# Kernel tuning notes

Measured on AMD Instinct MI355X. Metric: run time of the kernel, lower is better.

Reference implementation:

```python
import jax, jax.numpy as jnp
import numpy as np

FEATURE_SIZE = 128
STRIDE = 16
BASE_SIZE = 16
RATIOS = [0.5, 1, 2]
SCALES = [8, 16, 32]


def _generate_anchors(feature_size, stride):
    # Faithful to the torch module's numpy anchor generation (incl. rounding).
    size = BASE_SIZE * BASE_SIZE
    size_ratios = size / np.array(RATIOS)
    ws = np.round(np.sqrt(size_ratios))
    hs = np.round(ws * np.array(RATIOS))
    base = []
    for w, h in zip(ws, hs):
        for s in SCALES:
            base.append([0.0, 0.0, w * s, h * s])
    base = np.array(base)  # [9, 4]
    xo, yo = np.meshgrid(np.arange(feature_size), np.arange(feature_size), indexing='ij')
    # original loop order: x outer, y inner, then 9 base anchors
    centers = np.stack([xo * stride, yo * stride], axis=-1).reshape(-1, 1, 2)  # [F*F,1,2]
    wh = np.broadcast_to(base[None, :, 2:4], (feature_size * feature_size, 9, 2))
    anchors = np.concatenate([np.broadcast_to(centers, wh.shape), wh], axis=-1).reshape(-1, 4)
    return jnp.asarray(anchors, dtype=jnp.float32)  # [F*F*9, 4]


def _conv(x, w, b, pad):
    y = jax.lax.conv_general_dilated(
        x, w, window_strides=(1, 1), padding=[(pad, pad), (pad, pad)],
        dimension_numbers=('NCHW', 'OIHW', 'NCHW'))
    return y + b[None, :, None, None]


def setup_inputs() -> dict:
    key = jax.random.key(0)
    ks = jax.random.split(key, 4)
    F = FEATURE_SIZE
    x = jax.random.normal(ks[0], (1, 1024, F, F), dtype=jnp.float32)
    base_w = jax.random.normal(ks[1], (512, 1024, 3, 3), dtype=jnp.float32) * 0.01
    base_b = jnp.zeros((512,), dtype=jnp.float32)
    cls_w = jax.random.normal(ks[2], (18, 512, 1, 1), dtype=jnp.float32) * 0.01
    cls_b = jnp.zeros((18,), dtype=jnp.float32)
    reg_w = jax.random.normal(ks[3], (36, 512, 1, 1), dtype=jnp.float32) * 0.01
    reg_b = jnp.zeros((36,), dtype=jnp.float32)
    return {"x": x, "base_w": base_w, "base_b": base_b,
            "cls_w": cls_w, "cls_b": cls_b, "reg_w": reg_w, "reg_b": reg_b}


def reference(x, base_w, base_b, cls_w, cls_b, reg_w, reg_b):
    F = FEATURE_SIZE
    anchors = _generate_anchors(F, STRIDE)  # [N,4], N = F*F*9

    rpn_conv = jax.nn.relu(_conv(x, base_w, base_b, pad=1))        # [1,512,F,F]
    rpn_cls = _conv(rpn_conv, cls_w, cls_b, pad=0)                  # [1,18,F,F]
    # softmax over the 2-way fg/bg axis after reshape, as in the original
    cls_rs = rpn_cls.reshape(1, 2, 9 * F, F)
    cls_prob = jax.nn.softmax(cls_rs, axis=1).reshape(1, 18, F, F)
    rpn_reg = _conv(rpn_conv, reg_w, reg_b, pad=0)                  # [1,36,F,F]

    cls = jnp.transpose(cls_prob, (0, 2, 3, 1)).reshape(-1, 2)      # [N,2]
    reg = jnp.transpose(rpn_reg, (0, 2, 3, 1)).reshape(-1, 4)       # [N,4]

    # Vectorized decode — faithful to the original per-anchor loop math:
    # p0 = ax + aw*d0 ; p1 = ay + ah*d1 ; p2 = aw + exp(d2) ; p3 = ah + exp(d3)
    p0 = anchors[:, 0] + anchors[:, 2] * reg[:, 0]
    p1 = anchors[:, 1] + anchors[:, 3] * reg[:, 1]
    p2 = anchors[:, 2] + jnp.exp(reg[:, 2])
    p3 = anchors[:, 3] + jnp.exp(reg[:, 3])
    proposals = jnp.stack([p0, p1, p2, p3], axis=-1)                # [N,4]
    scores = cls[:, 1]                                              # [N]
    return jnp.concatenate([proposals, scores[:, None]], axis=-1)   # [N,5]
```

## Files before the change

kernel.cpp:

```cpp
#include <hip/hip_runtime.h>
#include <hip/hip_bf16.h>

typedef unsigned short u16;
typedef short s8v __attribute__((ext_vector_type(8)));
typedef float f4v __attribute__((ext_vector_type(4)));

#define F 128
#define CIN 1024
#define CMID 512
#define XP 130
#define K9 9216

#define A_ELEMS 8704
#define B_ELEMS 8192
#define AOFF(b) ((b) * A_ELEMS)
#define BOFF(b) (2 * A_ELEMS + (b) * B_ELEMS)

__device__ __forceinline__ u16 f2bf(float v) {
    union { float f; unsigned u; } x; x.f = v;
    unsigned r = x.u + 0x7fff + ((x.u >> 16) & 1);
    return (u16)(r >> 16);
}
__device__ __forceinline__ float bf2f(u16 u) {
    union { unsigned u; float f; } x; x.u = ((unsigned)u) << 16; return x.f;
}

__device__ __forceinline__ void gl16(const u16* g, u16* l) {
    __builtin_amdgcn_global_load_lds(
        (const __attribute__((address_space(1))) void*)g,
        (__attribute__((address_space(3))) void*)l,
        16, 0, 0);
}

__constant__ float WBASE[9] = {184.f, 368.f, 736.f, 128.f, 256.f, 512.f,  88.f, 176.f, 352.f};
__constant__ float HBASE[9] = { 96.f, 192.f, 384.f, 128.f, 256.f, 512.f, 176.f, 352.f, 704.f};

__global__ __launch_bounds__(256) void prep_all(
    const float* __restrict__ x, const float* __restrict__ bw,
    const float* __restrict__ cls_w, const float* __restrict__ reg_w,
    u16* __restrict__ xpad, u16* __restrict__ wt, u16* __restrict__ wc) {
    __shared__ char ldsraw[18624];
    const int b = blockIdx.x;
    const int tid = threadIdx.x;

    if (b < 258) {
        int t = b * 256 + tid;
        int cell = t >> 7, c8 = (t & 127) * 8;
        int h, w;
        if (cell < 130)      { h = 0;   w = cell; }
        else if (cell < 260) { h = 129; w = cell - 130; }
        else { int rm = cell - 260; h = 1 + (rm >> 1); w = (rm & 1) * 129; }
        s8v z = {};
        *(s8v*)&xpad[(h * XP + w) * CIN + c8] = z;
    } else if (b < 4354) {
        float (*lds)[65] = (float(*)[65])ldsraw;
        const int b2 = b - 258;
        const int h  = b2 >> 5;
        const int w0 = ((b2 >> 4) & 1) * 64;
        const int c0 = (b2 & 15) * 64;
        {
            const int wl = tid & 63, ci = tid >> 6;
            #pragma unroll
            for (int k = 0; k < 16; ++k) {
                int cl = ci * 16 + k;
                lds[cl][wl] = x[(c0 + cl) * (F * F) + h * F + (w0 + wl)];
            }
        }
        __syncthreads();
        {
            const int cs = (tid & 7) * 8;
            #pragma unroll
            for (int pass = 0; pass < 2; ++pass) {
                const int wl = (tid >> 3) + pass * 32;
                s8v v;
                #pragma unroll
                for (int j = 0; j < 8; ++j) v[j] = (short)f2bf(lds[cs + j][wl]);
                *(s8v*)&xpad[((h + 1) * XP + (w0 + wl + 1)) * CIN + c0 + cs] = v;
            }
        }
    } else if (b < 4866) {
        u16* lds = (u16*)ldsraw;
        const int oc = b - 4354;
        for (int k = 0; k < 36; ++k) {
            int idx = k * 256 + tid;
            float v = bw[oc * K9 + idx];
            int c = idx / 9, q = idx - c * 9;
            lds[q * 1033 + c] = f2bf(v);
        }
        __syncthreads();
        for (int k = 0; k < 36; ++k) {
            int idx = k * 256 + tid;
            int q = idx >> 10, c = idx & 1023;
            wt[oc * K9 + idx] = lds[q * 1033 + c];
        }
    } else {
        int t = (b - 4866) * 256 + tid;
        int oc = t >> 9, c = t & 511;
        float v = 0.f;
        if (oc < 18)      v = cls_w[oc * 512 + c];
        else if (oc < 54) v = reg_w[(oc - 18) * 512 + c];
        wc[t] = f2bf(v);
    }
}

__global__ __launch_bounds__(256, 2) void gemm_conv(
    const u16* __restrict__ xpad, const u16* __restrict__ wt,
    const float* __restrict__ bias, u16* __restrict__ rpn) {
    __shared__ u16 smem[2 * A_ELEMS + 2 * B_ELEMS];
    const int tid = threadIdx.x;
    const int bid = blockIdx.x;
    const int oc0 = ((bid & 7) >> 1) * 128;
    const int gh  = (bid >> 3) * 2 + (bid & 1);

    const int lane = tid & 63;
    const int wv = tid >> 6;
    const int lm = lane & 15;
    const int lq = lane >> 4;
    const int wm = (wv >> 1) * 64;
    const int wn = (wv & 1) * 64;

    const int sw = (lane & 7) ^ ((lane >> 3) & 7);
    const u16* pA = xpad + (lane >> 3) * CIN + sw * 8;
    const u16* pB = wt + (size_t)(oc0 + wv * 32 + (lane >> 3)) * K9 + sw * 8;

    f4v acc[4][4] = {};

    auto issueA = [&](int ms) {
        const int dy = ms >> 4, cc = ms & 15;
        const u16* src = pA + ((gh + dy) * XP) * CIN + cc * 64;
        u16* dst = &smem[AOFF(ms & 1)];
        #pragma unroll
        for (int jj = 0; jj < 4; ++jj) {
            const int ci = wv * 4 + jj;
            gl16(src + ci * 8 * CIN, dst + ci * 512);
        }
        if (wv == 0) gl16(src + 16 * 8 * CIN, dst + 16 * 512);
    };
    auto issueB = [&](int ms, int dx, int buf) {
        const int dy = ms >> 4, cc = ms & 15;
        const int dydx = dy * 3 + dx;
        const u16* src = pB + dydx * CIN + cc * 64;
        u16* dst = &smem[BOFF(buf) + wv * 32 * 64];
        #pragma unroll
        for (int jj = 0; jj < 4; ++jj)
            gl16(src + jj * 8 * K9, dst + jj * 8 * 64);
    };

    issueA(0);
    issueB(0, 0, 0);
    __syncthreads();

    int t = 0;
    for (int ms = 0; ms < 48; ++ms) {
        const u16* Ab = &smem[AOFF(ms & 1)];
        #pragma unroll
        for (int dx = 0; dx < 3; ++dx, ++t) {
            if (t + 1 < 144) {
                const int msn = (dx == 2) ? ms + 1 : ms;
                const int dxn = (dx == 2) ? 0 : dx + 1;
                issueB(msn, dxn, (t + 1) & 1);
            }
            if (dx == 0 && ms + 1 < 48) issueA(ms + 1);
            const u16* Bb = &smem[BOFF(t & 1)];
            #pragma unroll
            for (int kk = 0; kk < 2; ++kk) {
                const int kseg = kk * 4 + lq;
                s8v af[4], bfr[4];
                #pragma unroll
                for (int i = 0; i < 4; ++i) {
                    const int ra = wm + i * 16 + lm + dx;
                    const int rb = wn + i * 16 + lm;
                    af[i]  = *(const s8v*)&Ab[ra * 64 + ((kseg ^ (ra & 7)) << 3)];
                    bfr[i] = *(const s8v*)&Bb[rb * 64 + ((kseg ^ (rb & 7)) << 3)];
                }
                #pragma unroll
                for (int mi = 0; mi < 4; ++mi)
                    #pragma unroll
                    for (int ni = 0; ni < 4; ++ni)
                        acc[mi][ni] = __builtin_amdgcn_mfma_f32_16x16x32_bf16(
                            af[mi], bfr[ni], acc[mi][ni], 0, 0, 0);
            }
            __syncthreads();
        }
    }

    #pragma unroll
    for (int ni = 0; ni < 4; ++ni) {
        const int oc = oc0 + wn + ni * 16 + lm;
        const float bv = bias[oc];
        #pragma unroll
        for (int mi = 0; mi < 4; ++mi) {
            #pragma unroll
            for (int rr = 0; rr < 4; ++rr) {
                const int m = wm + mi * 16 + lq * 4 + rr;
                float v = acc[mi][ni][rr] + bv;
                v = v > 0.f ? v : 0.f;
                rpn[(gh * 128 + m) * CMID + oc] = f2bf(v);
            }
        }
    }
}

__global__ __launch_bounds__(256) void stage23(
    const u16* __restrict__ rpn, const u16* __restrict__ wc,
    const float* __restrict__ cls_b, const float* __restrict__ reg_b,
    float* __restrict__ out) {
    __shared__ float vals[64][65];
    const int tid = threadIdx.x, lane = tid & 63, wv = tid >> 6;
    const int lm = lane & 15, lq = lane >> 4;
    const int m0 = blockIdx.x * 64 + wv * 16;
    f4v acc[4] = {};
    const u16* arow = rpn + (m0 + lm) * CMID + lq * 8;
    const u16* brow = wc + lm * CMID + lq * 8;
    #pragma unroll
    for (int k = 0; k < 16; ++k) {
        s8v af = *(const s8v*)(arow + k * 32);
        #pragma unroll
        for (int ni = 0; ni < 4; ++ni) {
            s8v bf = *(const s8v*)(brow + ni * 16 * CMID + k * 32);
            acc[ni] = __builtin_amdgcn_mfma_f32_16x16x32_bf16(af, bf, acc[ni], 0, 0, 0);
        }
    }
    #pragma unroll
    for (int ni = 0; ni < 4; ++ni) {
        const int ch = ni * 16 + lm;
        const float bv = ch < 18 ? cls_b[ch] : (ch < 54 ? reg_b[ch - 18] : 0.f);
        #pragma unroll
        for (int rr = 0; rr < 4; ++rr)
            vals[wv * 16 + lq * 4 + rr][ch] = acc[ni][rr] + bv;
    }
    __syncthreads();
    const int pbase = blockIdx.x * 64;
    for (int q = tid; q < 576; q += 256) {
        const int pl = q / 9, a = q - pl * 9;
        const float* v = vals[pl];
        const int ch = 2 * a + 1;
        const int pair = (ch < 9) ? ch + 9 : ch - 9;
        const float score = 1.f / (1.f + expf(v[pair] - v[ch]));
        const float r0 = v[18 + 4 * a], r1 = v[19 + 4 * a];
        const float r2 = v[20 + 4 * a], r3 = v[21 + 4 * a];
        const float wb = WBASE[a], hb = HBASE[a];
        const int p = pbase + pl;
        const int h = p >> 7, w = p & 127;
        float* o = out + (p * 9 + a) * 5;
        o[0] = h * 16.f + wb * r0;
        o[1] = w * 16.f + hb * r1;
        o[2] = wb + expf(r2);
        o[3] = hb + expf(r3);
        o[4] = score;
    }
}

extern "C" void kernel_launch(void* const* d_in, const int* in_sizes, int n_in,
                              void* d_out, int out_size, void* d_ws, size_t ws_size,
                              hipStream_t stream) {
    const float* x      = (const float*)d_in[0];
    const float* base_w = (const float*)d_in[1];
    const float* base_b = (const float*)d_in[2];
    const float* cls_w  = (const float*)d_in[3];
    const float* cls_b  = (const float*)d_in[4];
    const float* reg_w  = (const float*)d_in[5];
    const float* reg_b  = (const float*)d_in[6];
    float* out = (float*)d_out;

    char* ws = (char*)d_ws;
    u16* xpad = (u16*)ws;
    u16* wt   = (u16*)(ws + 34611200);
    u16* wc   = (u16*)(ws + 34611200 + 9437184);
    u16* rpn  = (u16*)(ws + 34611200 + 9437184 + 65536);

    prep_all<<<4994, 256, 0, stream>>>(x, base_w, cls_w, reg_w, xpad, wt, wc);
    gemm_conv<<<512, 256, 0, stream>>>(xpad, wt, base_b, rpn);
    stage23<<<256, 256, 0, stream>>>(rpn, wc, cls_b, reg_b, out);
}
```

Baseline: 276.4 us.

## Load GEMM weight fragments directly from global memory, dropping LDS staging for B

The conv GEMM stops staging weight tiles in shared memory. Each lane now reads its B fragments straight from global memory into registers. This removes the B double buffer and cuts the barriers from three per input slice to one, and the smaller LDS footprint lets launch bounds rise to three blocks per SU. The input transpose prep kernel also switches to 16-byte vectorized float4 reads. The cost is that weight loads now sit on the critical path with global latency and no reuse across waves, and the higher occupancy target may force register spills.

```diff
diff --git a/kernel.cpp b/kernel.cpp
--- a/kernel.cpp
+++ b/kernel.cpp
@@ -12,9 +12,7 @@
 #define K9 9216
 
 #define A_ELEMS 8704
-#define B_ELEMS 8192
 #define AOFF(b) ((b) * A_ELEMS)
-#define BOFF(b) (2 * A_ELEMS + (b) * B_ELEMS)
 
 __device__ __forceinline__ u16 f2bf(float v) {
     union { float f; unsigned u; } x; x.f = v;
@@ -59,11 +57,14 @@
         const int w0 = ((b2 >> 4) & 1) * 64;
         const int c0 = (b2 & 15) * 64;
         {
-            const int wl = tid & 63, ci = tid >> 6;
-            #pragma unroll
-            for (int k = 0; k < 16; ++k) {
-                int cl = ci * 16 + k;
-                lds[cl][wl] = x[(c0 + cl) * (F * F) + h * F + (w0 + wl)];
+            const int c  = tid >> 2;
+            const int wq = tid & 3;
+            const float* src = x + (c0 + c) * (F * F) + h * F + w0 + wq * 16;
+            #pragma unroll
+            for (int k = 0; k < 4; ++k) {
+                f4v v = *(const f4v*)(src + k * 4);
+                #pragma unroll
+                for (int j = 0; j < 4; ++j) lds[c][wq * 16 + k * 4 + j] = v[j];
             }
         }
         __syncthreads();
@@ -103,10 +104,10 @@
     }
 }
 
-__global__ __launch_bounds__(256, 2) void gemm_conv(
+__global__ __launch_bounds__(256, 3) void gemm_conv(
     const u16* __restrict__ xpad, const u16* __restrict__ wt,
     const float* __restrict__ bias, u16* __restrict__ rpn) {
-    __shared__ u16 smem[2 * A_ELEMS + 2 * B_ELEMS];
+    __shared__ u16 smem[2 * A_ELEMS];
     const int tid = threadIdx.x;
     const int bid = blockIdx.x;
     const int oc0 = ((bid & 7) >> 1) * 128;
@@ -121,7 +122,7 @@
 
     const int sw = (lane & 7) ^ ((lane >> 3) & 7);
     const u16* pA = xpad + (lane >> 3) * CIN + sw * 8;
-    const u16* pB = wt + (size_t)(oc0 + wv * 32 + (lane >> 3)) * K9 + sw * 8;
+    const u16* pB = wt + (size_t)(oc0 + wn + lm) * K9 + lq * 8;
 
     f4v acc[4][4] = {};
 
@@ -136,42 +137,29 @@
         }
         if (wv == 0) gl16(src + 16 * 8 * CIN, dst + 16 * 512);
     };
-    auto issueB = [&](int ms, int dx, int buf) {
+
+    issueA(0);
+    __syncthreads();
+
+    for (int ms = 0; ms < 48; ++ms) {
         const int dy = ms >> 4, cc = ms & 15;
-        const int dydx = dy * 3 + dx;
-        const u16* src = pB + dydx * CIN + cc * 64;
-        u16* dst = &smem[BOFF(buf) + wv * 32 * 64];
-        #pragma unroll
-        for (int jj = 0; jj < 4; ++jj)
-            gl16(src + jj * 8 * K9, dst + jj * 8 * 64);
-    };
-
-    issueA(0);
-    issueB(0, 0, 0);
-    __syncthreads();
-
-    int t = 0;
-    for (int ms = 0; ms < 48; ++ms) {
+        if (ms + 1 < 48) issueA(ms + 1);
         const u16* Ab = &smem[AOFF(ms & 1)];
-        #pragma unroll
-        for (int dx = 0; dx < 3; ++dx, ++t) {
-            if (t + 1 < 144) {
-                const int msn = (dx == 2) ? ms + 1 : ms;
-                const int dxn = (dx == 2) ? 0 : dx + 1;
-                issueB(msn, dxn, (t + 1) & 1);
-            }
-            if (dx == 0 && ms + 1 < 48) issueA(ms + 1);
-            const u16* Bb = &smem[BOFF(t & 1)];
+        const u16* pBm = pB + (dy * 3) * CIN + cc * 64;
+        #pragma unroll
+        for (int dx = 0; dx < 3; ++dx) {
+            const u16* pBd = pBm + dx * CIN;
             #pragma unroll
             for (int kk = 0; kk < 2; ++kk) {
+                s8v af[4], bfr[4];
+                #pragma unroll
+                for (int i = 0; i < 4; ++i)
+                    bfr[i] = *(const s8v*)(pBd + (size_t)i * 16 * K9 + kk * 32);
                 const int kseg = kk * 4 + lq;
-                s8v af[4], bfr[4];
                 #pragma unroll
                 for (int i = 0; i < 4; ++i) {
                     const int ra = wm + i * 16 + lm + dx;
-                    const int rb = wn + i * 16 + lm;
-                    af[i]  = *(const s8v*)&Ab[ra * 64 + ((kseg ^ (ra & 7)) << 3)];
-                    bfr[i] = *(const s8v*)&Bb[rb * 64 + ((kseg ^ (rb & 7)) << 3)];
+                    af[i] = *(const s8v*)&Ab[ra * 64 + ((kseg ^ (ra & 7)) << 3)];
                 }
                 #pragma unroll
                 for (int mi = 0; mi < 4; ++mi)
@@ -180,8 +168,8 @@
                         acc[mi][ni] = __builtin_amdgcn_mfma_f32_16x16x32_bf16(
                             af[mi], bfr[ni], acc[mi][ni], 0, 0, 0);
             }
-            __syncthreads();
-        }
+        }
+        __syncthreads();
     }
 
     #pragma unroll
```

Measured after the change: 422.6 us. +52.9%, slower.

## Split prep kernel, vectorize x loads, and use split-K in stage23

Applied to the files above, without the earlier changes.

The fused prep kernel is split into separate x-transpose and weight-transpose kernels. This lets the x path use a smaller LDS footprint and 16-byte vectorized global loads. stage23 now splits the K=512 reduction across the 4 waves, reduces the partial sums through LDS, and launches 1024 blocks of 16 pixels instead of 256 blocks of 64, to expose more parallelism. The costs are an extra kernel launch and an extra LDS reduction with additional barriers.

```diff
diff --git a/kernel.cpp b/kernel.cpp
--- a/kernel.cpp
+++ b/kernel.cpp
@@ -35,11 +35,9 @@
 __constant__ float WBASE[9] = {184.f, 368.f, 736.f, 128.f, 256.f, 512.f,  88.f, 176.f, 352.f};
 __constant__ float HBASE[9] = { 96.f, 192.f, 384.f, 128.f, 256.f, 512.f, 176.f, 352.f, 704.f};
 
-__global__ __launch_bounds__(256) void prep_all(
-    const float* __restrict__ x, const float* __restrict__ bw,
-    const float* __restrict__ cls_w, const float* __restrict__ reg_w,
-    u16* __restrict__ xpad, u16* __restrict__ wt, u16* __restrict__ wc) {
-    __shared__ char ldsraw[18624];
+__global__ __launch_bounds__(256) void prep_x(
+    const float* __restrict__ x, u16* __restrict__ xpad) {
+    __shared__ float lds[64][65];
     const int b = blockIdx.x;
     const int tid = threadIdx.x;
 
@@ -52,35 +50,45 @@
         else { int rm = cell - 260; h = 1 + (rm >> 1); w = (rm & 1) * 129; }
         s8v z = {};
         *(s8v*)&xpad[(h * XP + w) * CIN + c8] = z;
-    } else if (b < 4354) {
-        float (*lds)[65] = (float(*)[65])ldsraw;
-        const int b2 = b - 258;
-        const int h  = b2 >> 5;
-        const int w0 = ((b2 >> 4) & 1) * 64;
-        const int c0 = (b2 & 15) * 64;
-        {
-            const int wl = tid & 63, ci = tid >> 6;
-            #pragma unroll
-            for (int k = 0; k < 16; ++k) {
-                int cl = ci * 16 + k;
-                lds[cl][wl] = x[(c0 + cl) * (F * F) + h * F + (w0 + wl)];
-            }
-        }
-        __syncthreads();
-        {
-            const int cs = (tid & 7) * 8;
-            #pragma unroll
-            for (int pass = 0; pass < 2; ++pass) {
-                const int wl = (tid >> 3) + pass * 32;
-                s8v v;
-                #pragma unroll
-                for (int j = 0; j < 8; ++j) v[j] = (short)f2bf(lds[cs + j][wl]);
-                *(s8v*)&xpad[((h + 1) * XP + (w0 + wl + 1)) * CIN + c0 + cs] = v;
-            }
-        }
-    } else if (b < 4866) {
-        u16* lds = (u16*)ldsraw;
-        const int oc = b - 4354;
+        return;
+    }
+    const int b2 = b - 258;
+    const int h  = b2 >> 5;
+    const int w0 = ((b2 >> 4) & 1) * 64;
+    const int c0 = (b2 & 15) * 64;
+    {
+        const int c  = tid >> 2;
+        const int wq = tid & 3;
+        const float* src = x + (c0 + c) * (F * F) + h * F + w0 + wq * 16;
+        #pragma unroll
+        for (int k = 0; k < 4; ++k) {
+            f4v v = *(const f4v*)(src + k * 4);
+            #pragma unroll
+            for (int j = 0; j < 4; ++j) lds[c][wq * 16 + k * 4 + j] = v[j];
+        }
+    }
+    __syncthreads();
+    {
+        const int cs = (tid & 7) * 8;
+        #pragma unroll
+        for (int pass = 0; pass < 2; ++pass) {
+            const int wl = (tid >> 3) + pass * 32;
+            s8v v;
+            #pragma unroll
+            for (int j = 0; j < 8; ++j) v[j] = (short)f2bf(lds[cs + j][wl]);
+            *(s8v*)&xpad[((h + 1) * XP + (w0 + wl + 1)) * CIN + c0 + cs] = v;
+        }
+    }
+}
+
+__global__ __launch_bounds__(256) void prep_w(
+    const float* __restrict__ bw, const float* __restrict__ cls_w,
+    const float* __restrict__ reg_w, u16* __restrict__ wt, u16* __restrict__ wc) {
+    __shared__ u16 lds[9 * 1033];
+    const int b = blockIdx.x;
+    const int tid = threadIdx.x;
+    if (b < 512) {
+        const int oc = b;
         for (int k = 0; k < 36; ++k) {
             int idx = k * 256 + tid;
             float v = bw[oc * K9 + idx];
@@ -94,7 +102,7 @@
             wt[oc * K9 + idx] = lds[q * 1033 + c];
         }
     } else {
-        int t = (b - 4866) * 256 + tid;
+        int t = (b - 512) * 256 + tid;
         int oc = t >> 9, c = t & 511;
         float v = 0.f;
         if (oc < 18)      v = cls_w[oc * 512 + c];
@@ -205,15 +213,16 @@
     const u16* __restrict__ rpn, const u16* __restrict__ wc,
     const float* __restrict__ cls_b, const float* __restrict__ reg_b,
     float* __restrict__ out) {
-    __shared__ float vals[64][65];
+    __shared__ float part[4][16][65];
     const int tid = threadIdx.x, lane = tid & 63, wv = tid >> 6;
     const int lm = lane & 15, lq = lane >> 4;
-    const int m0 = blockIdx.x * 64 + wv * 16;
+    const int m0 = blockIdx.x * 16;
+
     f4v acc[4] = {};
-    const u16* arow = rpn + (m0 + lm) * CMID + lq * 8;
-    const u16* brow = wc + lm * CMID + lq * 8;
-    #pragma unroll
-    for (int k = 0; k < 16; ++k) {
+    const u16* arow = rpn + (m0 + lm) * CMID + wv * 128 + lq * 8;
+    const u16* brow = wc + lm * CMID + wv * 128 + lq * 8;
+    #pragma unroll
+    for (int k = 0; k < 4; ++k) {
         s8v af = *(const s8v*)(arow + k * 32);
         #pragma unroll
         for (int ni = 0; ni < 4; ++ni) {
@@ -222,25 +231,37 @@
         }
     }
     #pragma unroll
-    for (int ni = 0; ni < 4; ++ni) {
-        const int ch = ni * 16 + lm;
-        const float bv = ch < 18 ? cls_b[ch] : (ch < 54 ? reg_b[ch - 18] : 0.f);
+    for (int ni = 0; ni < 4; ++ni)
         #pragma unroll
         for (int rr = 0; rr < 4; ++rr)
-            vals[wv * 16 + lq * 4 + rr][ch] = acc[ni][rr] + bv;
-    }
-    __syncthreads();
-    const int pbase = blockIdx.x * 64;
-    for (int q = tid; q < 576; q += 256) {
-        const int pl = q / 9, a = q - pl * 9;
-        const float* v = vals[pl];
+            part[wv][lq * 4 + rr][ni * 16 + lm] = acc[ni][rr];
+    __syncthreads();
+
+    float vsum[4];
+    const int col = tid & 63, rb = tid >> 6;
+    const float bv = col < 18 ? cls_b[col] : (col < 54 ? reg_b[col - 18] : 0.f);
+    #pragma unroll
+    for (int rr = 0; rr < 4; ++rr) {
+        const int row = rb * 4 + rr;
+        vsum[rr] = part[0][row][col] + part[1][row][col]
+                 + part[2][row][col] + part[3][row][col] + bv;
+    }
+    __syncthreads();
+    #pragma unroll
+    for (int rr = 0; rr < 4; ++rr)
+        part[0][rb * 4 + rr][col] = vsum[rr];
+    __syncthreads();
+
+    if (tid < 144) {
+        const int pl = tid / 9, a = tid - pl * 9;
+        const float* v = part[0][pl];
         const int ch = 2 * a + 1;
         const int pair = (ch < 9) ? ch + 9 : ch - 9;
         const float score = 1.f / (1.f + expf(v[pair] - v[ch]));
         const float r0 = v[18 + 4 * a], r1 = v[19 + 4 * a];
         const float r2 = v[20 + 4 * a], r3 = v[21 + 4 * a];
         const float wb = WBASE[a], hb = HBASE[a];
-        const int p = pbase + pl;
+        const int p = m0 + pl;
         const int h = p >> 7, w = p & 127;
         float* o = out + (p * 9 + a) * 5;
         o[0] = h * 16.f + wb * r0;
@@ -269,7 +290,8 @@
     u16* wc   = (u16*)(ws + 34611200 + 9437184);
     u16* rpn  = (u16*)(ws + 34611200 + 9437184 + 65536);
 
-    prep_all<<<4994, 256, 0, stream>>>(x, base_w, cls_w, reg_w, xpad, wt, wc);
+    prep_x<<<4354, 256, 0, stream>>>(x, xpad);
+    prep_w<<<640, 256, 0, stream>>>(base_w, cls_w, reg_w, wt, wc);
     gemm_conv<<<512, 256, 0, stream>>>(xpad, wt, base_b, rpn);
-    stage23<<<256, 256, 0, stream>>>(rpn, wc, cls_b, reg_b, out);
-}
+    stage23<<<1024, 256, 0, stream>>>(rpn, wc, cls_b, reg_b, out);
+}
```

After: 266.0 us. 1.04x faster.

## Fuse 1x1 head stage into conv GEMM via last-block atomic counter; vectorize x loads

Applied to the files above, without the earlier changes.

Removes the separate stage23 kernel. Each image row's four output-channel blocks bump an atomic counter, and the last one to finish runs the 1x1 cls/reg MFMA and the anchor decode for that row. Counters are zeroed by an extra block in the prep kernel. The x transpose load in prep also switches from scalar reads to float4 vector loads. The aim is to cut one launch and its tail, at the cost of serialising the head work onto the last-arriving blocks and adding threadfence/atomic overhead.

```diff
diff --git a/kernel.cpp b/kernel.cpp
--- a/kernel.cpp
+++ b/kernel.cpp
@@ -38,7 +38,8 @@
 __global__ __launch_bounds__(256) void prep_all(
     const float* __restrict__ x, const float* __restrict__ bw,
     const float* __restrict__ cls_w, const float* __restrict__ reg_w,
-    u16* __restrict__ xpad, u16* __restrict__ wt, u16* __restrict__ wc) {
+    u16* __restrict__ xpad, u16* __restrict__ wt, u16* __restrict__ wc,
+    int* __restrict__ cnt) {
     __shared__ char ldsraw[18624];
     const int b = blockIdx.x;
     const int tid = threadIdx.x;
@@ -59,11 +60,14 @@
         const int w0 = ((b2 >> 4) & 1) * 64;
         const int c0 = (b2 & 15) * 64;
         {
-            const int wl = tid & 63, ci = tid >> 6;
-            #pragma unroll
-            for (int k = 0; k < 16; ++k) {
-                int cl = ci * 16 + k;
-                lds[cl][wl] = x[(c0 + cl) * (F * F) + h * F + (w0 + wl)];
+            const int c  = tid >> 2;
+            const int wq = tid & 3;
+            const float* src = x + (c0 + c) * (F * F) + h * F + w0 + wq * 16;
+            #pragma unroll
+            for (int k = 0; k < 4; ++k) {
+                f4v v = *(const f4v*)(src + k * 4);
+                #pragma unroll
+                for (int j = 0; j < 4; ++j) lds[c][wq * 16 + k * 4 + j] = v[j];
             }
         }
         __syncthreads();
@@ -93,20 +97,26 @@
             int q = idx >> 10, c = idx & 1023;
             wt[oc * K9 + idx] = lds[q * 1033 + c];
         }
-    } else {
+    } else if (b < 4994) {
         int t = (b - 4866) * 256 + tid;
         int oc = t >> 9, c = t & 511;
         float v = 0.f;
         if (oc < 18)      v = cls_w[oc * 512 + c];
         else if (oc < 54) v = reg_w[(oc - 18) * 512 + c];
         wc[t] = f2bf(v);
+    } else {
+        if (tid < 128) cnt[tid] = 0;
     }
 }
 
 __global__ __launch_bounds__(256, 2) void gemm_conv(
     const u16* __restrict__ xpad, const u16* __restrict__ wt,
-    const float* __restrict__ bias, u16* __restrict__ rpn) {
+    const float* __restrict__ bias, u16* __restrict__ rpn,
+    const u16* __restrict__ wc, const float* __restrict__ cls_b,
+    const float* __restrict__ reg_b, float* __restrict__ out,
+    int* __restrict__ cnt) {
     __shared__ u16 smem[2 * A_ELEMS + 2 * B_ELEMS];
+    __shared__ int lastflag;
     const int tid = threadIdx.x;
     const int bid = blockIdx.x;
     const int oc0 = ((bid & 7) >> 1) * 128;
@@ -199,26 +209,25 @@
             }
         }
     }
-}
-
-__global__ __launch_bounds__(256) void stage23(
-    const u16* __restrict__ rpn, const u16* __restrict__ wc,
-    const float* __restrict__ cls_b, const float* __restrict__ reg_b,
-    float* __restrict__ out) {
-    __shared__ float vals[64][65];
-    const int tid = threadIdx.x, lane = tid & 63, wv = tid >> 6;
-    const int lm = lane & 15, lq = lane >> 4;
-    const int m0 = blockIdx.x * 64 + wv * 16;
-    f4v acc[4] = {};
-    const u16* arow = rpn + (m0 + lm) * CMID + lq * 8;
-    const u16* brow = wc + lm * CMID + lq * 8;
+
+    __threadfence();
+    if (tid == 0) lastflag = atomicAdd(&cnt[gh], 1);
+    __syncthreads();
+    if (lastflag != 3) return;
+    __threadfence();
+
+    float (*vals)[65] = (float(*)[65])smem;
+    const u16* rrow = rpn + (size_t)(gh * 128) * CMID;
+    f4v a2[2][4] = {};
     #pragma unroll
     for (int k = 0; k < 16; ++k) {
-        s8v af = *(const s8v*)(arow + k * 32);
+        s8v af0 = *(const s8v*)&rrow[(wv * 32 + lm) * CMID + k * 32 + lq * 8];
+        s8v af1 = *(const s8v*)&rrow[(wv * 32 + 16 + lm) * CMID + k * 32 + lq * 8];
         #pragma unroll
         for (int ni = 0; ni < 4; ++ni) {
-            s8v bf = *(const s8v*)(brow + ni * 16 * CMID + k * 32);
-            acc[ni] = __builtin_amdgcn_mfma_f32_16x16x32_bf16(af, bf, acc[ni], 0, 0, 0);
+            s8v bf = *(const s8v*)&wc[(ni * 16 + lm) * CMID + k * 32 + lq * 8];
+            a2[0][ni] = __builtin_amdgcn_mfma_f32_16x16x32_bf16(af0, bf, a2[0][ni], 0, 0, 0);
+            a2[1][ni] = __builtin_amdgcn_mfma_f32_16x16x32_bf16(af1, bf, a2[1][ni], 0, 0, 0);
         }
     }
     #pragma unroll
@@ -226,12 +235,13 @@
         const int ch = ni * 16 + lm;
         const float bv = ch < 18 ? cls_b[ch] : (ch < 54 ? reg_b[ch - 18] : 0.f);
         #pragma unroll
-        for (int rr = 0; rr < 4; ++rr)
-            vals[wv * 16 + lq * 4 + rr][ch] = acc[ni][rr] + bv;
+        for (int mi = 0; mi < 2; ++mi)
+            #pragma unroll
+            for (int rr = 0; rr < 4; ++rr)
+                vals[wv * 32 + mi * 16 + lq * 4 + rr][ch] = a2[mi][ni][rr] + bv;
     }
     __syncthreads();
-    const int pbase = blockIdx.x * 64;
-    for (int q = tid; q < 576; q += 256) {
+    for (int q = tid; q < 1152; q += 256) {
         const int pl = q / 9, a = q - pl * 9;
         const float* v = vals[pl];
         const int ch = 2 * a + 1;
@@ -240,7 +250,7 @@
         const float r0 = v[18 + 4 * a], r1 = v[19 + 4 * a];
         const float r2 = v[20 + 4 * a], r3 = v[21 + 4 * a];
         const float wb = WBASE[a], hb = HBASE[a];
-        const int p = pbase + pl;
+        const int p = gh * 128 + pl;
         const int h = p >> 7, w = p & 127;
         float* o = out + (p * 9 + a) * 5;
         o[0] = h * 16.f + wb * r0;
@@ -268,8 +278,9 @@
     u16* wt   = (u16*)(ws + 34611200);
     u16* wc   = (u16*)(ws + 34611200 + 9437184);
     u16* rpn  = (u16*)(ws + 34611200 + 9437184 + 65536);
-
-    prep_all<<<4994, 256, 0, stream>>>(x, base_w, cls_w, reg_w, xpad, wt, wc);
-    gemm_conv<<<512, 256, 0, stream>>>(xpad, wt, base_b, rpn);
-    stage23<<<256, 256, 0, stream>>>(rpn, wc, cls_b, reg_b, out);
-}
+    int* cnt  = (int*)(ws + 34611200 + 9437184 + 65536 + 16777216);
+
+    prep_all<<<4995, 256, 0, stream>>>(x, base_w, cls_w, reg_w, xpad, wt, wc, cnt);
+    gemm_conv<<<512, 256, 0, stream>>>(xpad, wt, base_b, rpn,
+                                       wc, cls_b, reg_b, out, cnt);
+}
```

After: 398.3 us. +44.1%, slower.
